# Kernel tuning notes

Hardware: AMD Instinct MI355X
Metric: run time of the kernel (lower is better)

Reference implementation:

```python
import jax, jax.numpy as jnp
import numpy as np

# Module hyperparameters (init_kwargs)
N_CLASSES = 21
RADIUS = 5
SIZE = (256, 256)
SIGMA_DIST = 4.0
SIGMA_FEAT = 1.0
B, C = 8, 32


def _offsets(radius):
    """Integer (dy, dx) offsets with Euclidean distance < radius (includes (0,0))."""
    offs = []
    r = int(radius)
    for dy in range(-r + 1, r):
        for dx in range(-r + 1, r):
            if dy * dy + dx * dx < radius * radius:
                offs.append((dy, dx))
    return offs


OFFSETS = _offsets(RADIUS)  # 69 offsets for radius=5


def setup_inputs() -> dict:
    key = jax.random.key(0)
    k1, k2 = jax.random.split(key)
    H, W = SIZE
    classification = jax.random.uniform(k1, (B, N_CLASSES, H, W), dtype=jnp.float32)
    features = jax.random.normal(k2, (B, C, H, W), dtype=jnp.float32)
    return {"classification": classification, "features": features}


def reference(classification, features):
    # classification: [B, K, H, W] soft assignments S
    # features:       [B, C, H, W]
    Bb, K, H, W = classification.shape
    inv_sd2 = 1.0 / (SIGMA_DIST * SIGMA_DIST)
    inv_sf2 = 1.0 / (SIGMA_FEAT * SIGMA_FEAT)

    hs = jnp.arange(H)
    ws = jnp.arange(W)

    WS = jnp.zeros_like(classification)           # (W @ S), [B, K, H, W]
    degree = jnp.zeros((Bb, H, W), classification.dtype)

    # Loop over the small fixed set of neighbor offsets (69 for radius=5).
    for dy, dx in OFFSETS:
        f_nb = jnp.roll(features, (-dy, -dx), axis=(2, 3))
        s_nb = jnp.roll(classification, (-dy, -dx), axis=(2, 3))
        # mask out wrap-around: neighbor (h+dy, w+dx) must be in-bounds
        valid_h = (hs + dy >= 0) & (hs + dy < H)
        valid_w = (ws + dx >= 0) & (ws + dx < W)
        mask = (valid_h[:, None] & valid_w[None, :]).astype(classification.dtype)
        # Gaussian affinity: distance kernel * feature kernel
        feat_d2 = ((features - f_nb) ** 2).sum(axis=1)        # [B, H, W]
        w = jnp.exp(-(dy * dy + dx * dx) * inv_sd2 - feat_d2 * inv_sf2) * mask
        WS = WS + w[:, None] * s_nb
        degree = degree + w

    # numerator   = S^T W S : [B, K, K]
    # denominator = d^T S   : [B, K]
    num = jnp.einsum('bkhw,bjhw->bkj', classification, WS)
    den = jnp.einsum('bhw,bkhw->bk', degree, classification)
    return (num / den[:, None, :]).sum()
```

## Files before the change

kernel.cpp:

```cpp
#include <hip/hip_runtime.h>

#define HH 256
#define WW 256
#define HWPX 65536
#define BB 8
#define KK 21
#define CC 32

typedef _Float16 half2v __attribute__((ext_vector_type(2)));
union F4H { float4 f4; half2v h[4]; };

__global__ __launch_bounds__(256) void prep(const float* __restrict__ cls,
                                            const float* __restrict__ feat,
                                            float4* __restrict__ fpk,
                                            float2* __restrict__ TN) {
    const int tid = blockIdx.x * 256 + threadIdx.x;
    const int b = tid >> 16;
    const int p = tid & (HWPX - 1);

    const float* cbase = cls + (size_t)b * KK * HWPX + p;
    float T = 0.f;
#pragma unroll
    for (int k = 0; k < KK; ++k) T += cbase[(size_t)k * HWPX];

    const float* src = feat + (size_t)b * CC * HWPX + p;
    float nq = 0.f;
#pragma unroll
    for (int j = 0; j < 4; ++j) {
        F4H u;
#pragma unroll
        for (int k = 0; k < 4; ++k) {
            float a  = src[(size_t)(j * 8 + 2 * k) * HWPX];
            float b2 = src[(size_t)(j * 8 + 2 * k + 1) * HWPX];
            u.h[k] = __builtin_bit_cast(half2v, __builtin_amdgcn_cvt_pkrtz(a, b2));
            nq = __builtin_amdgcn_fdot2(u.h[k], u.h[k], nq, false);
        }
        fpk[(size_t)j * (BB * HWPX) + tid] = u.f4;
    }
    TN[tid] = make_float2(T, nq);
}

__global__ __launch_bounds__(256, 4) void affinity4(const float4* __restrict__ fpk,
                                                    const float2* __restrict__ TN,
                                                    const float* __restrict__ cls,
                                                    float* __restrict__ numer,
                                                    float* __restrict__ denom) {
    __shared__ float smN[4][22], smD[4][22];
    const int L  = blockIdx.x;
    const int b  = L & 7;
    const int t  = L >> 3;
    const int by = t & 15;
    const int bx = (t >> 4) & 3;
    const int half = t >> 6;
    const int lane = threadIdx.x & 63;
    const int wid  = threadIdx.x >> 6;
    const int gx  = bx * 64 + lane;
    const int gy0 = by * 16 + wid * 4;

    const size_t bofs = (size_t)b * HWPX;
    const float4* fb0 = fpk + bofs;
    const float4* fb1 = fpk + (size_t)1 * BB * HWPX + bofs;
    const float4* fb2 = fpk + (size_t)2 * BB * HWPX + bofs;
    const float4* fb3 = fpk + (size_t)3 * BB * HWPX + bofs;
    const float2* tnb = TN + bofs;

    F4H fp[4][4];
    float np_[4];
#pragma unroll
    for (int py = 0; py < 4; ++py) {
        const int pp = ((gy0 + py) << 8) | gx;
        fp[py][0].f4 = fb0[pp];
        fp[py][1].f4 = fb1[pp];
        fp[py][2].f4 = fb2[pp];
        fp[py][3].f4 = fb3[pp];
        np_[py] = tnb[pp].y;
    }

    float degacc[4] = {0.f, 0.f, 0.f, 0.f};
    float vacc[4]   = {0.f, 0.f, 0.f, 0.f};

    const int dy_lo = half * 6;
    const int dy_hi = dy_lo + 6;

#pragma unroll 1
    for (int dyi = dy_lo; dyi < dy_hi; ++dyi) {
        const int ny = gy0 + dyi - 4;
        if ((unsigned)ny >= HH) continue;
        const int rowq = ny << 8;

        int dy2[4];
        float base[4];
#pragma unroll
        for (int py = 0; py < 4; ++py) {
            const int d = dyi - 4 - py;
            dy2[py] = d * d;
            base[py] = fmaf(-0.03125f, (float)dy2[py], -0.5f * np_[py]);
        }
        const int mind = min(min(dy2[0], dy2[1]), min(dy2[2], dy2[3]));

#pragma unroll 3
        for (int dxi = 0; dxi < 9; ++dxi) {
            const int dx = dxi - 4;
            const int dx2 = dx * dx;
            if (mind + dx2 >= 25) continue;

            const int gx2 = gx + dx;
            const bool vx = (unsigned)gx2 < WW;
            const int q = rowq | min(max(gx2, 0), WW - 1);

            F4H nb0, nb1, nb2, nb3;
            nb0.f4 = fb0[q];
            nb1.f4 = fb1[q];
            nb2.f4 = fb2[q];
            nb3.f4 = fb3[q];
            const float2 tq = tnb[q];
            const float cdx = (float)dx2 * -0.03125f;

#pragma unroll
            for (int py = 0; py < 4; ++py) {
                if (dy2[py] + dx2 < 25) {
                    float c0 = fmaf(-0.5f, tq.y, base[py] + cdx);
                    float c1 = 0.f, c2 = 0.f, c3 = 0.f;
#pragma unroll
                    for (int k = 0; k < 4; ++k) {
                        c0 = __builtin_amdgcn_fdot2(fp[py][0].h[k], nb0.h[k], c0, false);
                        c1 = __builtin_amdgcn_fdot2(fp[py][1].h[k], nb1.h[k], c1, false);
                        c2 = __builtin_amdgcn_fdot2(fp[py][2].h[k], nb2.h[k], c2, false);
                        c3 = __builtin_amdgcn_fdot2(fp[py][3].h[k], nb3.h[k], c3, false);
                    }
                    const float acc = (c0 + c1) + (c2 + c3);
                    float w = __builtin_exp2f(acc * 2.8853900817779268f);
                    w = vx ? w : 0.f;
                    degacc[py] += w;
                    vacc[py] = fmaf(w, tq.x, vacc[py]);
                }
            }
        }
    }

    const float* clsb = cls + (size_t)b * KK * HWPX;
#pragma unroll 1
    for (int jc = 0; jc < 3; ++jc) {
        float accN[7], accD[7];
#pragma unroll
        for (int jj = 0; jj < 7; ++jj) {
            const float* cj = clsb + (size_t)(jc * 7 + jj) * HWPX;
            float n = 0.f, d = 0.f;
#pragma unroll
            for (int py = 0; py < 4; ++py) {
                const float s = cj[((gy0 + py) << 8) | gx];
                n = fmaf(s, vacc[py], n);
                d = fmaf(s, degacc[py], d);
            }
            accN[jj] = n; accD[jj] = d;
        }
#pragma unroll
        for (int jj = 0; jj < 7; ++jj) {
            float n = accN[jj], d = accD[jj];
#pragma unroll
            for (int off = 32; off > 0; off >>= 1) {
                n += __shfl_down(n, off);
                d += __shfl_down(d, off);
            }
            if (lane == 0) { smN[wid][jc * 7 + jj] = n; smD[wid][jc * 7 + jj] = d; }
        }
    }
    __syncthreads();
    if (threadIdx.x < 2 * KK) {
        const int h2 = threadIdx.x / KK;
        const int j = threadIdx.x - h2 * KK;
        const float a = h2 ? (smD[0][j] + smD[1][j] + smD[2][j] + smD[3][j])
                           : (smN[0][j] + smN[1][j] + smN[2][j] + smN[3][j]);
        atomicAdd((h2 ? denom : numer) + b * KK + j, a);
    }
}

__global__ __launch_bounds__(256) void finalize(const float* __restrict__ numer,
                                                const float* __restrict__ denom,
                                                float* __restrict__ out) {
    __shared__ float sm[4];
    int i = threadIdx.x;
    float r = 0.f;
    if (i < BB * KK) r = numer[i] / denom[i];
#pragma unroll
    for (int off = 32; off > 0; off >>= 1) r += __shfl_down(r, off);
    if ((i & 63) == 0) sm[i >> 6] = r;
    __syncthreads();
    if (i == 0) out[0] = sm[0] + sm[1] + sm[2] + sm[3];
}

extern "C" void kernel_launch(void* const* d_in, const int* in_sizes, int n_in,
                              void* d_out, int out_size, void* d_ws, size_t ws_size,
                              hipStream_t stream) {
    const float* cls  = (const float*)d_in[0];
    const float* feat = (const float*)d_in[1];
    float* out = (float*)d_out;

    const size_t BHW = (size_t)BB * HWPX;
    float4* fpk  = (float4*)d_ws;
    float2* TN   = (float2*)((char*)d_ws + BHW * 64);
    float*  numer = (float*)((char*)TN + BHW * 8);
    float*  denom = numer + BB * KK;

    (void)hipMemsetAsync(numer, 0, 2 * BB * KK * sizeof(float), stream);
    prep<<<dim3((BB * HWPX) / 256), dim3(256), 0, stream>>>(cls, feat, fpk, TN);
    affinity4<<<dim3(1024), dim3(256), 0, stream>>>(fpk, TN, cls, numer, denom);
    finalize<<<dim3(1), dim3(256), 0, stream>>>(numer, denom, out);
}
```

Baseline: 198.8 us.

## Compute neighbor feature dot products with MFMA 16x16x32 tiles

Replaces the per-pixel fdot2 loop with a matrix-core formulation: each wave takes a 16-pixel row segment and computes the full 16x16 dot-product block against two 16-wide neighbor windows per dy using mfma_f32_16x16x32_f16. Entries outside the radius are masked after the exp. The atomicAdd accumulation is replaced by a per-block partial buffer plus a separate reduction kernel, which also removes the memset. This trades some redundant work (the full 16x32 window per row instead of only in-radius offsets) for matrix-core throughput, and adds an extra launch.

```diff
diff --git a/kernel.cpp b/kernel.cpp
--- a/kernel.cpp
+++ b/kernel.cpp
@@ -6,9 +6,13 @@
 #define BB 8
 #define KK 21
 #define CC 32
+#define NT 8192
+#define E_LOG2E 1.4426950408889634f
 
 typedef _Float16 half2v __attribute__((ext_vector_type(2)));
-union F4H { float4 f4; half2v h[4]; };
+typedef _Float16 half8  __attribute__((ext_vector_type(8)));
+typedef float    f32x4v __attribute__((ext_vector_type(4)));
+union F4H { float4 f4; half2v h[4]; half8 h8; };
 
 __global__ __launch_bounds__(256) void prep(const float* __restrict__ cls,
                                             const float* __restrict__ feat,
@@ -40,138 +44,146 @@
     TN[tid] = make_float2(T, nq);
 }
 
-__global__ __launch_bounds__(256, 4) void affinity4(const float4* __restrict__ fpk,
-                                                    const float2* __restrict__ TN,
-                                                    const float* __restrict__ cls,
-                                                    float* __restrict__ numer,
-                                                    float* __restrict__ denom) {
-    __shared__ float smN[4][22], smD[4][22];
-    const int L  = blockIdx.x;
-    const int b  = L & 7;
-    const int t  = L >> 3;
-    const int by = t & 15;
-    const int bx = (t >> 4) & 3;
-    const int half = t >> 6;
+__global__ __launch_bounds__(256) void affinity_mfma(const float4* __restrict__ fpk,
+                                                     const float2* __restrict__ TN,
+                                                     const float* __restrict__ cls,
+                                                     float* __restrict__ partial) {
+    __shared__ float smN[4][21], smD[4][21];
+    const int L    = blockIdx.x;
+    const int b    = L & 7;
+    const int t    = L >> 3;
+    const int xt   = t >> 6;
+    const int ygrp = t & 63;
+    const int wid  = threadIdx.x >> 6;
     const int lane = threadIdx.x & 63;
-    const int wid  = threadIdx.x >> 6;
-    const int gx  = bx * 64 + lane;
-    const int gy0 = by * 16 + wid * 4;
+    const int g    = lane >> 4;
+    const int c    = lane & 15;
+    const int y    = ygrp * 4 + wid;
+    const int x0   = xt * 16;
 
     const size_t bofs = (size_t)b * HWPX;
-    const float4* fb0 = fpk + bofs;
-    const float4* fb1 = fpk + (size_t)1 * BB * HWPX + bofs;
-    const float4* fb2 = fpk + (size_t)2 * BB * HWPX + bofs;
-    const float4* fb3 = fpk + (size_t)3 * BB * HWPX + bofs;
+    const float4* fb  = fpk + bofs;
     const float2* tnb = TN + bofs;
 
-    F4H fp[4][4];
-    float np_[4];
-#pragma unroll
-    for (int py = 0; py < 4; ++py) {
-        const int pp = ((gy0 + py) << 8) | gx;
-        fp[py][0].f4 = fb0[pp];
-        fp[py][1].f4 = fb1[pp];
-        fp[py][2].f4 = fb2[pp];
-        fp[py][3].f4 = fb3[pp];
-        np_[py] = tnb[pp].y;
-    }
-
-    float degacc[4] = {0.f, 0.f, 0.f, 0.f};
-    float vacc[4]   = {0.f, 0.f, 0.f, 0.f};
-
-    const int dy_lo = half * 6;
-    const int dy_hi = dy_lo + 6;
+    const int rowp = (y << 8) + x0;
+    F4H afr; afr.f4 = fb[(size_t)g * (BB * HWPX) + rowp + c];
+
+    float npE[4];
+#pragma unroll
+    for (int r = 0; r < 4; ++r) npE[r] = tnb[rowp + 4 * g + r].y * E_LOG2E;
+
+    int   swr[2][4];
+    float cst[2][4];
+#pragma unroll
+    for (int w = 0; w < 2; ++w) {
+        const int w0  = w ? 12 : -4;
+        const int xbu = x0 + w0 + c;
+        const bool inb = (unsigned)xbu < WW;
+#pragma unroll
+        for (int r = 0; r < 4; ++r) {
+            const int dx = w0 + c - 4 * g - r;
+            swr[w][r] = inb ? dx * dx : 999;
+            cst[w][r] = fmaf((float)(dx * dx), -E_LOG2E / 16.f, -npE[r]);
+        }
+    }
+
+    float pdeg[4] = {0.f, 0.f, 0.f, 0.f};
+    float pV[4]   = {0.f, 0.f, 0.f, 0.f};
 
 #pragma unroll 1
-    for (int dyi = dy_lo; dyi < dy_hi; ++dyi) {
-        const int ny = gy0 + dyi - 4;
+    for (int dyi = 0; dyi < 9; ++dyi) {
+        const int ny = y + dyi - 4;
         if ((unsigned)ny >= HH) continue;
-        const int rowq = ny << 8;
-
-        int dy2[4];
-        float base[4];
-#pragma unroll
-        for (int py = 0; py < 4; ++py) {
-            const int d = dyi - 4 - py;
-            dy2[py] = d * d;
-            base[py] = fmaf(-0.03125f, (float)dy2[py], -0.5f * np_[py]);
-        }
-        const int mind = min(min(dy2[0], dy2[1]), min(dy2[2], dy2[3]));
-
-#pragma unroll 3
-        for (int dxi = 0; dxi < 9; ++dxi) {
-            const int dx = dxi - 4;
-            const int dx2 = dx * dx;
-            if (mind + dx2 >= 25) continue;
-
-            const int gx2 = gx + dx;
-            const bool vx = (unsigned)gx2 < WW;
-            const int q = rowq | min(max(gx2, 0), WW - 1);
-
-            F4H nb0, nb1, nb2, nb3;
-            nb0.f4 = fb0[q];
-            nb1.f4 = fb1[q];
-            nb2.f4 = fb2[q];
-            nb3.f4 = fb3[q];
+        const int dy2  = (dyi - 4) * (dyi - 4);
+        const float cdy = (float)dy2 * (-E_LOG2E / 16.f);
+        const int thr  = 25 - dy2;
+        const int nrow = ny << 8;
+
+#pragma unroll
+        for (int w = 0; w < 2; ++w) {
+            const int w0  = w ? 12 : -4;
+            const int xbc = min(max(x0 + w0 + c, 0), WW - 1);
+            const int q   = nrow + xbc;
+
+            F4H bfr; bfr.f4 = fb[(size_t)g * (BB * HWPX) + q];
             const float2 tq = tnb[q];
-            const float cdx = (float)dx2 * -0.03125f;
-
-#pragma unroll
-            for (int py = 0; py < 4; ++py) {
-                if (dy2[py] + dx2 < 25) {
-                    float c0 = fmaf(-0.5f, tq.y, base[py] + cdx);
-                    float c1 = 0.f, c2 = 0.f, c3 = 0.f;
-#pragma unroll
-                    for (int k = 0; k < 4; ++k) {
-                        c0 = __builtin_amdgcn_fdot2(fp[py][0].h[k], nb0.h[k], c0, false);
-                        c1 = __builtin_amdgcn_fdot2(fp[py][1].h[k], nb1.h[k], c1, false);
-                        c2 = __builtin_amdgcn_fdot2(fp[py][2].h[k], nb2.h[k], c2, false);
-                        c3 = __builtin_amdgcn_fdot2(fp[py][3].h[k], nb3.h[k], c3, false);
-                    }
-                    const float acc = (c0 + c1) + (c2 + c3);
-                    float w = __builtin_exp2f(acc * 2.8853900817779268f);
-                    w = vx ? w : 0.f;
-                    degacc[py] += w;
-                    vacc[py] = fmaf(w, tq.x, vacc[py]);
-                }
+
+            f32x4v cz = {0.f, 0.f, 0.f, 0.f};
+            cz = __builtin_amdgcn_mfma_f32_16x16x32_f16(afr.h8, bfr.h8, cz, 0, 0, 0);
+
+            const float t1 = fmaf(tq.y, -E_LOG2E, cdy);
+#pragma unroll
+            for (int r = 0; r < 4; ++r) {
+                const float e2 = fmaf(cz[r], 2.f * E_LOG2E, cst[w][r] + t1);
+                float wv = __builtin_exp2f(e2);
+                wv = (swr[w][r] < thr) ? wv : 0.f;
+                pdeg[r] += wv;
+                pV[r]   = fmaf(wv, tq.x, pV[r]);
             }
         }
     }
 
-    const float* clsb = cls + (size_t)b * KK * HWPX;
-#pragma unroll 1
-    for (int jc = 0; jc < 3; ++jc) {
-        float accN[7], accD[7];
-#pragma unroll
-        for (int jj = 0; jj < 7; ++jj) {
-            const float* cj = clsb + (size_t)(jc * 7 + jj) * HWPX;
-            float n = 0.f, d = 0.f;
-#pragma unroll
-            for (int py = 0; py < 4; ++py) {
-                const float s = cj[((gy0 + py) << 8) | gx];
-                n = fmaf(s, vacc[py], n);
-                d = fmaf(s, degacc[py], d);
-            }
-            accN[jj] = n; accD[jj] = d;
-        }
-#pragma unroll
-        for (int jj = 0; jj < 7; ++jj) {
-            float n = accN[jj], d = accD[jj];
-#pragma unroll
-            for (int off = 32; off > 0; off >>= 1) {
-                n += __shfl_down(n, off);
-                d += __shfl_down(d, off);
-            }
-            if (lane == 0) { smN[wid][jc * 7 + jj] = n; smD[wid][jc * 7 + jj] = d; }
-        }
+#pragma unroll
+    for (int m = 1; m <= 8; m <<= 1) {
+#pragma unroll
+        for (int r = 0; r < 4; ++r) {
+            pdeg[r] += __shfl_xor(pdeg[r], m, 64);
+            pV[r]   += __shfl_xor(pV[r], m, 64);
+        }
+    }
+
+    float n0 = 0.f, d0 = 0.f, n1 = 0.f, d1 = 0.f;
+    const float* clsb = cls + (size_t)b * KK * HWPX + rowp + 4 * g;
+#pragma unroll
+    for (int r = 0; r < 4; ++r) {
+        const float s0 = clsb[(size_t)c * HWPX + r];
+        n0 = fmaf(s0, pV[r], n0);
+        d0 = fmaf(s0, pdeg[r], d0);
+        if (c < 5) {
+            const float s1 = clsb[(size_t)(c + 16) * HWPX + r];
+            n1 = fmaf(s1, pV[r], n1);
+            d1 = fmaf(s1, pdeg[r], d1);
+        }
+    }
+#pragma unroll
+    for (int m = 16; m <= 32; m <<= 1) {
+        n0 += __shfl_xor(n0, m, 64);
+        d0 += __shfl_xor(d0, m, 64);
+        n1 += __shfl_xor(n1, m, 64);
+        d1 += __shfl_xor(d1, m, 64);
+    }
+    if (lane < 16) {
+        smN[wid][lane] = n0;
+        smD[wid][lane] = d0;
+        if (lane < 5) { smN[wid][16 + lane] = n1; smD[wid][16 + lane] = d1; }
     }
     __syncthreads();
     if (threadIdx.x < 2 * KK) {
-        const int h2 = threadIdx.x / KK;
-        const int j = threadIdx.x - h2 * KK;
-        const float a = h2 ? (smD[0][j] + smD[1][j] + smD[2][j] + smD[3][j])
-                           : (smN[0][j] + smN[1][j] + smN[2][j] + smN[3][j]);
-        atomicAdd((h2 ? denom : numer) + b * KK + j, a);
+        const int jq = threadIdx.x;
+        const float v = (jq < KK)
+            ? (smN[0][jq] + smN[1][jq] + smN[2][jq] + smN[3][jq])
+            : (smD[0][jq - KK] + smD[1][jq - KK] + smD[2][jq - KK] + smD[3][jq - KK]);
+        partial[(size_t)jq * NT + (size_t)b * 1024 + t] = v;
+    }
+}
+
+__global__ __launch_bounds__(256) void reduce_part(const float* __restrict__ partial,
+                                                   float* __restrict__ numer,
+                                                   float* __restrict__ denom) {
+    __shared__ float sm[4];
+    const int jq = blockIdx.x;
+    const int b  = blockIdx.y;
+    const float* src = partial + (size_t)jq * NT + (size_t)b * 1024;
+    float a = src[threadIdx.x] + src[threadIdx.x + 256]
+            + src[threadIdx.x + 512] + src[threadIdx.x + 768];
+#pragma unroll
+    for (int off = 32; off > 0; off >>= 1) a += __shfl_down(a, off);
+    if ((threadIdx.x & 63) == 0) sm[threadIdx.x >> 6] = a;
+    __syncthreads();
+    if (threadIdx.x == 0) {
+        const float v = sm[0] + sm[1] + sm[2] + sm[3];
+        if (jq < KK) numer[b * KK + jq] = v;
+        else         denom[b * KK + jq - KK] = v;
     }
 }
 
@@ -197,13 +209,14 @@
     float* out = (float*)d_out;
 
     const size_t BHW = (size_t)BB * HWPX;
-    float4* fpk  = (float4*)d_ws;
-    float2* TN   = (float2*)((char*)d_ws + BHW * 64);
-    float*  numer = (float*)((char*)TN + BHW * 8);
-    float*  denom = numer + BB * KK;
-
-    (void)hipMemsetAsync(numer, 0, 2 * BB * KK * sizeof(float), stream);
+    float4* fpk     = (float4*)d_ws;
+    float2* TN      = (float2*)((char*)d_ws + BHW * 64);
+    float*  partial = (float*)((char*)TN + BHW * 8);
+    float*  numer   = partial + (size_t)2 * KK * NT;
+    float*  denom   = numer + BB * KK;
+
     prep<<<dim3((BB * HWPX) / 256), dim3(256), 0, stream>>>(cls, feat, fpk, TN);
-    affinity4<<<dim3(1024), dim3(256), 0, stream>>>(fpk, TN, cls, numer, denom);
+    affinity_mfma<<<dim3(NT), dim3(256), 0, stream>>>(fpk, TN, cls, partial);
+    reduce_part<<<dim3(2 * KK, BB), dim3(256), 0, stream>>>(partial, numer, denom);
     finalize<<<dim3(1), dim3(256), 0, stream>>>(numer, denom, out);
 }
```

After: 206.8 us. +4.0%, slower.
